# Kernel tuning notes

Measured on AMD Instinct MI355X. Metric: run time of the kernel, lower is better.

Reference implementation:

```python
import jax, jax.numpy as jnp
import numpy as np

N_NODES = 4096
NUM_GRAPHS = 16
NODE_DIM = 8
EDGE_DIM = 4
HID = 128
N_WIRES = 9  # 3 edge wires + 4 node wires (center=3) + 2 ancillas
SEL_LAYERS = 1
PI = np.pi


def _c(x):
    return x.astype(jnp.complex64)


def _ry(t):
    c, s = _c(jnp.cos(t / 2)), _c(jnp.sin(t / 2))
    return jnp.stack([jnp.stack([c, -s], -1), jnp.stack([s, c], -1)], -2)


def _rx(t):
    c, s = _c(jnp.cos(t / 2)), -1j * _c(jnp.sin(t / 2))
    return jnp.stack([jnp.stack([c, s], -1), jnp.stack([s, c], -1)], -2)


def _rz(t):
    e = jnp.exp(-0.5j * _c(t))
    z = jnp.zeros_like(e)
    return jnp.stack([jnp.stack([e, z], -1), jnp.stack([z, jnp.conj(e)], -1)], -2)


def _rot(phi, theta, omega):  # qml.Rot = RZ(omega) @ RY(theta) @ RZ(phi)
    return _rz(omega) @ _ry(theta) @ _rz(phi)


def _ctrl(U):  # block-diag(I2, U)
    b = U.shape[:-2]
    I = jnp.broadcast_to(jnp.eye(2, dtype=jnp.complex64), b + (2, 2))
    Z = jnp.zeros(b + (2, 2), jnp.complex64)
    return jnp.concatenate([jnp.concatenate([I, Z], -1), jnp.concatenate([Z, U], -1)], -2)


_CNOT = jnp.array([[1, 0, 0, 0], [0, 1, 0, 0], [0, 0, 0, 1], [0, 0, 1, 0]], jnp.complex64)


def _apply1(state, U, w):  # state [S, 2**9], U [2,2] or [S,2,2]
    S = state.shape[0]
    s = jnp.moveaxis(state.reshape((S,) + (2,) * N_WIRES), 1 + w, 1)
    out = jnp.einsum('bij,bjk->bik', jnp.broadcast_to(U, (S, 2, 2)), s.reshape(S, 2, -1))
    return jnp.moveaxis(out.reshape(s.shape), 1, 1 + w).reshape(S, -1)


def _apply2(state, U, w1, w2):  # U [4,4] or [S,4,4], wire order (w1,w2)
    S = state.shape[0]
    s = jnp.moveaxis(state.reshape((S,) + (2,) * N_WIRES), (1 + w1, 1 + w2), (1, 2))
    out = jnp.einsum('bij,bjk->bik', jnp.broadcast_to(U, (S, 4, 4)), s.reshape(S, 4, -1))
    return jnp.moveaxis(out.reshape(s.shape), (1, 2), (1 + w1, 1 + w2)).reshape(S, -1)


def _sel(state, weights, wires):  # qml.StronglyEntanglingLayers, weights [L, n, 3]->here [L,3,3]
    L, n = weights.shape[0], len(wires)
    for l in range(L):
        for j, w in enumerate(wires):
            state = _apply1(state, _rot(weights[l, j, 0], weights[l, j, 1], weights[l, j, 2]), w)
        r = l % (n - 1) + 1
        for j in range(n):
            state = _apply2(state, _CNOT, wires[j], wires[(j + r) % n])
    return state


def _pqc(inputs, strong, inits, update):
    # inputs: [S, 7, 2] angles (rows 0..2 edge feats, rows 3..6 node feats, center node = row 3)
    S = inputs.shape[0]
    state = jnp.zeros((S, 2 ** N_WIRES), jnp.complex64).at[:, 0].set(1.0)
    for i in range(3):
        state = _apply1(state, _ry(inputs[:, i, 0]), i)
        state = _apply1(state, _rz(inputs[:, i, 1]), i)
    for i in range(4):
        state = _apply1(state, _ry(inputs[:, 3 + i, 0]), 3 + i)
        state = _apply1(state, _rz(inputs[:, 3 + i, 1]), 3 + i)
    for i in range(3):  # message_passing_pqc per edge
        e, nb, a1, a2 = i, 4 + i, 7, 8
        state = _apply2(state, _ctrl(_rx(inits[0, 0])), nb, a1)
        state = _apply2(state, _ctrl(_ry(inits[0, 1])), e, a1)
        state = _apply2(state, _ctrl(_rz(inits[0, 2])), nb, a2)
        state = _apply2(state, _ctrl(_ry(inits[0, 3])), e, a2)
        state = _sel(state, strong[0], [e, nb, a1])
        state = _sel(state, strong[1], [a1, nb, a2])
    state = _sel(state, update, [3, 7, 8])
    # expval(PauliX) on center wire 3: wires 0..2 -> 8, wire 3 -> 2, wires 4..8 -> 32
    s = state.reshape(S, 8, 2, 32)
    return 2.0 * jnp.real(jnp.sum(jnp.conj(s[:, :, 0]) * s[:, :, 1], axis=(1, 2)))


def _mlp(x, W1, b1, W2, b2):  # PyG MLP, act between layers, dropout in eval = identity
    return jax.nn.leaky_relu(x @ W1 + b1) @ W2 + b2


def _forward(node_feat, edge_attr, Wn1, bn1, Wn2, bn2, We1, be1, We2, be2,
             strong, inits, update, Wu1, bu1, Wu2, bu2, Wh1, bh1, Wh2, bh2,
             subgraphs, edge_ids, batch):
    x = jnp.tanh(_mlp(node_feat, Wn1, bn1, Wn2, bn2)) * PI   # input_process
    e = jnp.tanh(_mlp(edge_attr, We1, be1, We2, be2)) * PI
    q_in = jnp.concatenate([e[edge_ids], x[subgraphs]], axis=1)  # [S,3,2]+[S,4,2] -> [S,7,2]
    aggr = _pqc(q_in, strong, inits, update)[:, None]            # [S,1]
    centers = subgraphs[:, 0]
    upd = _mlp(jnp.concatenate([x[centers], aggr], axis=-1), Wu1, bu1, Wu2, bu2)  # [S,2]
    x = x + jnp.zeros_like(x).at[centers].add(upd)               # index_add + residual
    gsum = jax.ops.segment_sum(x, batch, num_segments=NUM_GRAPHS)
    gcnt = jax.ops.segment_sum(jnp.ones((x.shape[0], 1), x.dtype), batch, num_segments=NUM_GRAPHS)
    g = gsum / gcnt                                              # global_mean_pool
    return _mlp(g, Wh1, bh1, Wh2, bh2)


def setup_inputs() -> dict:
    key = jax.random.key(0)
    ks = jax.random.split(key, 16)
    N, G = N_NODES, NUM_GRAPHS
    node_feat = jax.random.normal(ks[0], (N, NODE_DIM), jnp.float32)
    edge_attr = jax.random.normal(ks[1], (3 * N, EDGE_DIM), jnp.float32)
    i = np.arange(N)
    # star subgraph per node: center i with ring neighbors i+1,i+2,i+3 (mod N);
    # edge (i, i+k) has id 3*i + (k-1) in edge_attr (idx_dict materialized).
    subgraphs = jnp.asarray(np.stack([i, (i + 1) % N, (i + 2) % N, (i + 3) % N], 1), jnp.int32)
    edge_ids = jnp.asarray(np.stack([3 * i, 3 * i + 1, 3 * i + 2], 1), jnp.int32)
    batch = jnp.asarray(i // (N // G), jnp.int32)

    def lin(k, fan_in, shape):
        return jax.random.uniform(k, shape, jnp.float32, -1.0, 1.0) / np.sqrt(fan_in)

    def qw(k, shape):  # uniform_pi_init
        return jax.random.uniform(k, shape, jnp.float32, 0.0, PI)

    k = jax.random.split(ks[2], 24)
    return {
        'node_feat': node_feat, 'edge_attr': edge_attr,
        'Wn1': lin(k[0], NODE_DIM, (NODE_DIM, HID)), 'bn1': lin(k[1], NODE_DIM, (HID,)),
        'Wn2': lin(k[2], HID, (HID, 2)), 'bn2': lin(k[3], HID, (2,)),
        'We1': lin(k[4], EDGE_DIM, (EDGE_DIM, HID)), 'be1': lin(k[5], EDGE_DIM, (HID,)),
        'We2': lin(k[6], HID, (HID, 2)), 'be2': lin(k[7], HID, (2,)),
        'strong': qw(k[8], (2, SEL_LAYERS, 3, 3)), 'inits': qw(k[9], (1, 4)),
        'update': qw(k[10], (SEL_LAYERS, 3, 3)),
        'Wu1': lin(k[11], 3, (3, HID)), 'bu1': lin(k[12], 3, (HID,)),
        'Wu2': lin(k[13], HID, (HID, 2)), 'bu2': lin(k[14], HID, (2,)),
        'Wh1': lin(k[15], 2, (2, 2)), 'bh1': lin(k[16], 2, (2,)),
        'Wh2': lin(k[17], 2, (2, 2)), 'bh2': lin(k[18], 2, (2,)),
        'subgraphs': subgraphs, 'edge_ids': edge_ids, 'batch': batch,
    }


def reference(node_feat, edge_attr, Wn1, bn1, Wn2, bn2, We1, be1, We2, be2,
              strong, inits, update, Wu1, bu1, Wu2, bu2, Wh1, bh1, Wh2, bh2,
              subgraphs, edge_ids, batch):
    return _forward(node_feat, edge_attr, Wn1, bn1, Wn2, bn2, We1, be1, We2, be2,
                    strong, inits, update, Wu1, bu1, Wu2, bu2, Wh1, bh1, Wh2, bh2,
                    subgraphs, edge_ids, batch)
```

## Files before the change

kernel.cpp:

```cpp
#include <hip/hip_runtime.h>
#include <math.h>

#define PI_F 3.14159265358979323846f

__device__ __forceinline__ float2 cmul2(float2 a, float2 b) {
    return make_float2(a.x * b.x - a.y * b.y, a.x * b.y + a.y * b.x);
}
__device__ __forceinline__ float2 cmac2(float2 u, float2 a, float2 v, float2 b) {
    float2 r;
    r.x = u.x * a.x - u.y * a.y + v.x * b.x - v.y * b.y;
    r.y = u.x * a.y + u.y * a.x + v.x * b.y + v.y * b.x;
    return r;
}

struct M4 { float2 u00, u01, u10, u11; };

__device__ __forceinline__ M4 mmul4(const M4& A, const M4& B) {
    M4 R;
    R.u00 = cmac2(A.u00, B.u00, A.u01, B.u10);
    R.u01 = cmac2(A.u00, B.u01, A.u01, B.u11);
    R.u10 = cmac2(A.u10, B.u00, A.u11, B.u10);
    R.u11 = cmac2(A.u10, B.u01, A.u11, B.u11);
    return R;
}
__device__ __forceinline__ M4 mry(float t) {
    float c = cosf(0.5f * t), s = sinf(0.5f * t);
    M4 R; R.u00 = {c, 0}; R.u01 = {-s, 0}; R.u10 = {s, 0}; R.u11 = {c, 0};
    return R;
}
__device__ __forceinline__ M4 mrz(float t) {
    float c = cosf(0.5f * t), s = sinf(0.5f * t);
    M4 R; R.u00 = {c, -s}; R.u01 = {0, 0}; R.u10 = {0, 0}; R.u11 = {c, s};
    return R;
}
__device__ __forceinline__ M4 mrx(float t) {
    float c = cosf(0.5f * t), s = sinf(0.5f * t);
    M4 R; R.u00 = {c, 0}; R.u01 = {0, -s}; R.u10 = {0, -s}; R.u11 = {c, 0};
    return R;
}
__device__ __forceinline__ M4 mrot(float phi, float th, float om) {
    return mmul4(mmul4(mrz(om), mry(th)), mrz(phi));
}

__device__ __forceinline__ float2 shflx(float2 v, int mask) {
    return make_float2(__shfl_xor(v.x, mask, 64), __shfl_xor(v.y, mask, 64));
}

__device__ __forceinline__ M4 ldm(const float* __restrict__ g) {
    M4 M;
    M.u00 = make_float2(g[0], g[1]); M.u01 = make_float2(g[2], g[3]);
    M.u10 = make_float2(g[4], g[5]); M.u11 = make_float2(g[6], g[7]);
    return M;
}


template <int TB>
__device__ __forceinline__ void rot_reg(const M4& U, float2 (&amp)[8]) {
#pragma unroll
    for (int r = 0; r < 8; r++)
        if (((r >> TB) & 1) == 0) {
            int r1 = r | (1 << TB);
            float2 a = amp[r], b = amp[r1];
            amp[r]  = cmac2(U.u00, a, U.u01, b);
            amp[r1] = cmac2(U.u10, a, U.u11, b);
        }
}

template <int LB>
__device__ __forceinline__ void rot_lane(const M4& U, float2 (&amp)[8], int lane) {
    bool hi = (lane >> LB) & 1;
    float2 cA = hi ? U.u11 : U.u00;
    float2 cB = hi ? U.u10 : U.u01;
#pragma unroll
    for (int r = 0; r < 8; r++) {
        float2 o = shflx(amp[r], 1 << LB);
        amp[r] = cmac2(cA, amp[r], cB, o);
    }
}

template <int WIRE>
__device__ __forceinline__ void rot1(const M4& U, float2 (&amp)[8], int lane) {
    constexpr int BIT = 8 - WIRE;
    if constexpr (BIT < 3) rot_reg<BIT>(U, amp);
    else rot_lane<BIT - 3>(U, amp, lane);
}

template <int CW, int TW>
__device__ __forceinline__ void crot(const M4& U, float2 (&amp)[8], int lane) {
    constexpr int CBIT = 8 - CW, TBIT = 8 - TW;
    static_assert(TBIT < 3, "controlled targets are reg bits here");
    if constexpr (CBIT >= 3) {
        bool c = (lane >> (CBIT - 3)) & 1;
        M4 E;
        E.u00 = c ? U.u00 : make_float2(1.f, 0.f);
        E.u01 = c ? U.u01 : make_float2(0.f, 0.f);
        E.u10 = c ? U.u10 : make_float2(0.f, 0.f);
        E.u11 = c ? U.u11 : make_float2(1.f, 0.f);
        rot_reg<TBIT>(E, amp);
    } else {
#pragma unroll
        for (int r = 0; r < 8; r++)
            if (((r >> CBIT) & 1) == 1 && ((r >> TBIT) & 1) == 0) {
                int r1 = r | (1 << TBIT);
                float2 a = amp[r], b = amp[r1];
                amp[r]  = cmac2(U.u00, a, U.u01, b);
                amp[r1] = cmac2(U.u10, a, U.u11, b);
            }
    }
}

template <int CW, int TW>
__device__ __forceinline__ void cnotg(float2 (&amp)[8], int lane) {
    constexpr int CBIT = 8 - CW, TBIT = 8 - TW;
    if constexpr (CBIT < 3 && TBIT < 3) {
#pragma unroll
        for (int r = 0; r < 8; r++)
            if (((r >> CBIT) & 1) == 1 && ((r >> TBIT) & 1) == 0) {
                int r1 = r | (1 << TBIT);
                float2 t = amp[r]; amp[r] = amp[r1]; amp[r1] = t;
            }
    } else if constexpr (CBIT >= 3 && TBIT < 3) {
        bool c = (lane >> (CBIT - 3)) & 1;
#pragma unroll
        for (int r = 0; r < 8; r++)
            if (((r >> TBIT) & 1) == 0) {
                int r1 = r | (1 << TBIT);
                float2 t0 = amp[r], t1 = amp[r1];
                amp[r]  = c ? t1 : t0;
                amp[r1] = c ? t0 : t1;
            }
    } else if constexpr (CBIT < 3 && TBIT >= 3) {
#pragma unroll
        for (int r = 0; r < 8; r++)
            if (((r >> CBIT) & 1) == 1) {
                amp[r] = shflx(amp[r], 1 << (TBIT - 3));
            }
    } else {
        bool c = (lane >> (CBIT - 3)) & 1;
#pragma unroll
        for (int r = 0; r < 8; r++) {
            float2 o = shflx(amp[r], 1 << (TBIT - 3));
            amp[r] = c ? o : amp[r];
        }
    }
}

template <int W0, int W1, int W2>
__device__ __forceinline__ void sel3m(const float* __restrict__ gm, float2 (&amp)[8], int lane) {
    rot1<W0>(ldm(gm),      amp, lane);
    rot1<W1>(ldm(gm + 8),  amp, lane);
    rot1<W2>(ldm(gm + 16), amp, lane);
    cnotg<W0, W1>(amp, lane);
    cnotg<W1, W2>(amp, lane);
    cnotg<W2, W0>(amp, lane);
}

template <int I>
__device__ __forceinline__ void block_i(float2 (&amp)[8], const M4& crx, const M4& cry1,
                                        const M4& crz, const M4& cry2,
                                        const float* __restrict__ gm, int lane) {
    constexpr int EW = I, NB = 4 + I;
    crot<NB, 7>(crx,  amp, lane);
    crot<EW, 7>(cry1, amp, lane);
    crot<NB, 8>(crz,  amp, lane);
    crot<EW, 8>(cry2, amp, lane);
    sel3m<EW, NB, 7>(gm + 32, amp, lane);
    sel3m<7, NB, 8>(gm + 56,  amp, lane);
}


__global__ void prep_kernel(const float* __restrict__ strong, const float* __restrict__ inits,
                            const float* __restrict__ update, float* __restrict__ gm) {
    int j = threadIdx.x;
    if (j >= 13) return;
    M4 M;
    if (j == 0)      M = mrx(inits[0]);
    else if (j == 1) M = mry(inits[1]);
    else if (j == 2) M = mrz(inits[2]);
    else if (j == 3) M = mry(inits[3]);
    else if (j < 7)  { const float* w = strong + (j - 4) * 3;     M = mrot(w[0], w[1], w[2]); }
    else if (j < 10) { const float* w = strong + 9 + (j - 7) * 3; M = mrot(w[0], w[1], w[2]); }
    else             { const float* w = update + (j - 10) * 3;    M = mrot(w[0], w[1], w[2]); }
    float* o = gm + j * 8;
    o[0] = M.u00.x; o[1] = M.u00.y; o[2] = M.u01.x; o[3] = M.u01.y;
    o[4] = M.u10.x; o[5] = M.u10.y; o[6] = M.u11.x; o[7] = M.u11.y;
}

__global__ __launch_bounds__(256) void mlp_both_kernel(
        const float* __restrict__ node_feat, const float* __restrict__ edge_attr,
        const float* __restrict__ Wn1, const float* __restrict__ bn1,
        const float* __restrict__ Wn2, const float* __restrict__ bn2,
        const float* __restrict__ We1, const float* __restrict__ be1,
        const float* __restrict__ We2, const float* __restrict__ be2,
        float* __restrict__ x, float* __restrict__ e,
        int N, int NE, int nodeBlocks) {
    if ((int)blockIdx.x < nodeBlocks) {
        int r = blockIdx.x * 256 + threadIdx.x;
        if (r >= N) return;
        float f[8];
#pragma unroll
        for (int k = 0; k < 8; k++) f[k] = node_feat[r * 8 + k];
        float o0 = bn2[0], o1 = bn2[1];
        for (int j = 0; j < 128; j++) {
            float h = bn1[j];
#pragma unroll
            for (int k = 0; k < 8; k++) h += f[k] * Wn1[k * 128 + j];
            h = h > 0.f ? h : 0.01f * h;
            o0 += h * Wn2[j * 2 + 0];
            o1 += h * Wn2[j * 2 + 1];
        }
        x[r * 2 + 0] = tanhf(o0) * PI_F;
        x[r * 2 + 1] = tanhf(o1) * PI_F;
    } else {
        int r = (blockIdx.x - nodeBlocks) * 256 + threadIdx.x;
        if (r >= NE) return;
        float f[4];
#pragma unroll
        for (int k = 0; k < 4; k++) f[k] = edge_attr[r * 4 + k];
        float o0 = be2[0], o1 = be2[1];
        for (int j = 0; j < 128; j++) {
            float h = be1[j];
#pragma unroll
            for (int k = 0; k < 4; k++) h += f[k] * We1[k * 128 + j];
            h = h > 0.f ? h : 0.01f * h;
            o0 += h * We2[j * 2 + 0];
            o1 += h * We2[j * 2 + 1];
        }
        e[r * 2 + 0] = tanhf(o0) * PI_F;
        e[r * 2 + 1] = tanhf(o1) * PI_F;
    }
}

__global__ __launch_bounds__(256) void pqc_kernel(
        const float* __restrict__ x, const float* __restrict__ e,
        const int* __restrict__ subgraphs, const int* __restrict__ edge_ids,
        const float* __restrict__ gm, float* __restrict__ aggr, int ntot) {
    int wave = threadIdx.x >> 6;
    int lane = threadIdx.x & 63;
    int s = blockIdx.x * 4 + wave;
    if (s >= ntot) return;

    float ang[7][2];
    for (int j = 0; j < 3; j++) {
        int eid = edge_ids[s * 3 + j];
        ang[j][0] = e[2 * eid]; ang[j][1] = e[2 * eid + 1];
    }
    for (int j = 0; j < 4; j++) {
        int nid = subgraphs[s * 4 + j];
        ang[3 + j][0] = x[2 * nid]; ang[3 + j][1] = x[2 * nid + 1];
    }

    float2 c = make_float2(1.f, 0.f);
#pragma unroll
    for (int w = 0; w < 6; w++) {
        float a = 0.5f * ang[w][0], b = 0.5f * ang[w][1];
        float ca = __cosf(a), sa = __sinf(a);
        float cb = __cosf(b), sb = __sinf(b);
        float2 v0 = make_float2(ca * cb, -ca * sb);
        float2 v1 = make_float2(sa * cb,  sa * sb);
        int bit = (lane >> (5 - w)) & 1;
        c = cmul2(c, bit ? v1 : v0);
    }
    float2 amp[8];
#pragma unroll
    for (int r = 0; r < 8; r++) amp[r] = make_float2(0.f, 0.f);
    {
        float a = 0.5f * ang[6][0], b = 0.5f * ang[6][1];
        float ca = __cosf(a), sa = __sinf(a);
        float cb = __cosf(b), sb = __sinf(b);
        amp[0] = cmul2(c, make_float2(ca * cb, -ca * sb));
        amp[4] = cmul2(c, make_float2(sa * cb,  sa * sb));
    }

    M4 crx  = ldm(gm);
    M4 cry1 = ldm(gm + 8);
    M4 crz  = ldm(gm + 16);
    M4 cry2 = ldm(gm + 24);

    block_i<0>(amp, crx, cry1, crz, cry2, gm, lane);
    block_i<1>(amp, crx, cry1, crz, cry2, gm, lane);
    block_i<2>(amp, crx, cry1, crz, cry2, gm, lane);
    sel3m<3, 7, 8>(gm + 80, amp, lane);

    float acc = 0.f;
#pragma unroll
    for (int r = 0; r < 8; r++) {
        float2 o = shflx(amp[r], 4);
        acc += amp[r].x * o.x + amp[r].y * o.y;
    }
    for (int off = 32; off > 0; off >>= 1) acc += __shfl_down(acc, off, 64);
    if (lane == 0) aggr[s] = acc;
}

__global__ void upd_kernel(const float* __restrict__ x, const float* __restrict__ aggr,
                           const int* __restrict__ subgraphs,
                           const float* __restrict__ W1, const float* __restrict__ b1,
                           const float* __restrict__ W2, const float* __restrict__ b2,
                           float* __restrict__ xadd, int rows) {
    int r = blockIdx.x * blockDim.x + threadIdx.x;
    if (r >= rows) return;
    int c = subgraphs[r * 4];
    float f0 = x[2 * c], f1 = x[2 * c + 1], f2 = aggr[r];
    float o0 = b2[0], o1 = b2[1];
    for (int j = 0; j < 128; j++) {
        float h = b1[j] + f0 * W1[j] + f1 * W1[128 + j] + f2 * W1[256 + j];
        h = h > 0.f ? h : 0.01f * h;
        o0 += h * W2[j * 2 + 0];
        o1 += h * W2[j * 2 + 1];
    }
    atomicAdd(&xadd[2 * c + 0], o0);
    atomicAdd(&xadd[2 * c + 1], o1);
}

#define MAX_GRAPHS 64
__global__ __launch_bounds__(256) void pool_kernel(
        const float* __restrict__ x, const float* __restrict__ xadd,
        const int* __restrict__ batch,
        float* __restrict__ gsum, float* __restrict__ gcnt, int rows, int ngraphs) {
    __shared__ float bins[3 * MAX_GRAPHS];
    for (int i = threadIdx.x; i < 3 * ngraphs; i += blockDim.x) bins[i] = 0.f;
    __syncthreads();

    int r = blockIdx.x * blockDim.x + threadIdx.x;
    int lane = threadIdx.x & 63;
    bool active = r < rows;
    int b = 0; float v0 = 0.f, v1 = 0.f, cc = 0.f;
    if (active) {
        b = batch[r];
        v0 = x[2 * r + 0] + xadd[2 * r + 0];
        v1 = x[2 * r + 1] + xadd[2 * r + 1];
        cc = 1.f;
    }
    int b0 = __shfl(b, 0);
    bool uni = __all(active && b == b0);
    if (uni) {
        for (int off = 32; off > 0; off >>= 1) {
            v0 += __shfl_down(v0, off);
            v1 += __shfl_down(v1, off);
        }
        if (lane == 0) {
            atomicAdd(&bins[3 * b0 + 0], v0);
            atomicAdd(&bins[3 * b0 + 1], v1);
            atomicAdd(&bins[3 * b0 + 2], 64.f);
        }
    } else if (active) {
        atomicAdd(&bins[3 * b + 0], v0);
        atomicAdd(&bins[3 * b + 1], v1);
        atomicAdd(&bins[3 * b + 2], cc);
    }
    __syncthreads();

    for (int i = threadIdx.x; i < ngraphs; i += blockDim.x) {
        float s0 = bins[3 * i + 0], s1 = bins[3 * i + 1], sc = bins[3 * i + 2];
        if (s0 != 0.f || s1 != 0.f || sc != 0.f) {
            atomicAdd(&gsum[2 * i + 0], s0);
            atomicAdd(&gsum[2 * i + 1], s1);
            atomicAdd(&gcnt[i], sc);
        }
    }
}

__global__ void head_kernel(const float* __restrict__ gsum, const float* __restrict__ gcnt,
                            const float* __restrict__ Wh1, const float* __restrict__ bh1,
                            const float* __restrict__ Wh2, const float* __restrict__ bh2,
                            float* __restrict__ out, int ngraphs) {
    int g = threadIdx.x;
    if (g >= ngraphs) return;
    float c = gcnt[g];
    float g0 = gsum[2 * g + 0] / c;
    float g1 = gsum[2 * g + 1] / c;
    float h0 = g0 * Wh1[0] + g1 * Wh1[2] + bh1[0];
    float h1 = g0 * Wh1[1] + g1 * Wh1[3] + bh1[1];
    h0 = h0 > 0.f ? h0 : 0.01f * h0;
    h1 = h1 > 0.f ? h1 : 0.01f * h1;
    out[2 * g + 0] = h0 * Wh2[0] + h1 * Wh2[2] + bh2[0];
    out[2 * g + 1] = h0 * Wh2[1] + h1 * Wh2[3] + bh2[1];
}

extern "C" void kernel_launch(void* const* d_in, const int* in_sizes, int n_in,
                              void* d_out, int out_size, void* d_ws, size_t ws_size,
                              hipStream_t stream) {
    const float* node_feat = (const float*)d_in[0];
    const float* edge_attr = (const float*)d_in[1];
    const float* Wn1 = (const float*)d_in[2];
    const float* bn1 = (const float*)d_in[3];
    const float* Wn2 = (const float*)d_in[4];
    const float* bn2 = (const float*)d_in[5];
    const float* We1 = (const float*)d_in[6];
    const float* be1 = (const float*)d_in[7];
    const float* We2 = (const float*)d_in[8];
    const float* be2 = (const float*)d_in[9];
    const float* strong = (const float*)d_in[10];
    const float* inits  = (const float*)d_in[11];
    const float* update = (const float*)d_in[12];
    const float* Wu1 = (const float*)d_in[13];
    const float* bu1 = (const float*)d_in[14];
    const float* Wu2 = (const float*)d_in[15];
    const float* bu2 = (const float*)d_in[16];
    const float* Wh1 = (const float*)d_in[17];
    const float* bh1 = (const float*)d_in[18];
    const float* Wh2 = (const float*)d_in[19];
    const float* bh2 = (const float*)d_in[20];
    const int* subgraphs = (const int*)d_in[21];
    const int* edge_ids  = (const int*)d_in[22];
    const int* batch     = (const int*)d_in[23];

    const int N  = in_sizes[0] / 8;
    const int NE = in_sizes[1] / 4;
    const int NG = out_size / 2;

    float* ws   = (float*)d_ws;
    float* x    = ws;
    float* e    = x + (size_t)N * 2;
    float* aggr = e + (size_t)NE * 2;
    float* xadd = aggr + N;
    float* gsum = xadd + (size_t)N * 2;
    float* gcnt = gsum + (size_t)NG * 2;
    float* gm   = gcnt + NG;

    hipMemsetAsync(xadd, 0, (size_t)(N * 2 + NG * 3) * sizeof(float), stream);

    prep_kernel<<<1, 64, 0, stream>>>(strong, inits, update, gm);

    int nodeBlocks = (N + 255) / 256;
    int edgeBlocks = (NE + 255) / 256;
    mlp_both_kernel<<<nodeBlocks + edgeBlocks, 256, 0, stream>>>(
        node_feat, edge_attr, Wn1, bn1, Wn2, bn2, We1, be1, We2, be2, x, e, N, NE, nodeBlocks);

    pqc_kernel<<<(N + 3) / 4, 256, 0, stream>>>(x, e, subgraphs, edge_ids, gm, aggr, N);

    upd_kernel<<<(N + 255) / 256, 256, 0, stream>>>(x, aggr, subgraphs, Wu1, bu1, Wu2, bu2, xadd, N);
    pool_kernel<<<(N + 255) / 256, 256, 0, stream>>>(x, xadd, batch, gsum, gcnt, N, NG);
    head_kernel<<<1, 64, 0, stream>>>(gsum, gcnt, Wh1, bh1, Wh2, bh2, (float*)d_out, NG);
}
```

Baseline: 162.7 us.

## Fuse update MLP into pooling, specialize controlled rotations, fold memset into prep

The separate update kernel that scattered into an xadd buffer is merged into the pooling kernel, which now adds each row's update output straight into the graph bin of its center node. This removes the xadd buffer, one launch and the memset. The small zeroing of gsum/gcnt moves into prep_kernel. Controlled RX/RY/RZ gates now use specialized real cos/sin arithmetic instead of generic complex 2x2 matrices, which cuts FLOPs in the PQC kernel. The fused path relies on the center node being in the same graph for the warp-uniform fast path; otherwise it falls back to per-thread shared atomics.

Measured after the change: 151.2 us. -7.0%, faster.

```diff
diff --git a/kernel.cpp b/kernel.cpp
--- a/kernel.cpp
+++ b/kernel.cpp
@@ -33,11 +33,6 @@
     M4 R; R.u00 = {c, -s}; R.u01 = {0, 0}; R.u10 = {0, 0}; R.u11 = {c, s};
     return R;
 }
-__device__ __forceinline__ M4 mrx(float t) {
-    float c = cosf(0.5f * t), s = sinf(0.5f * t);
-    M4 R; R.u00 = {c, 0}; R.u01 = {0, -s}; R.u10 = {0, -s}; R.u11 = {c, 0};
-    return R;
-}
 __device__ __forceinline__ M4 mrot(float phi, float th, float om) {
     return mmul4(mmul4(mrz(om), mry(th)), mrz(phi));
 }
@@ -85,26 +80,78 @@
     else rot_lane<BIT - 3>(U, amp, lane);
 }
 
-template <int CW, int TW>
-__device__ __forceinline__ void crot(const M4& U, float2 (&amp)[8], int lane) {
-    constexpr int CBIT = 8 - CW, TBIT = 8 - TW;
-    static_assert(TBIT < 3, "controlled targets are reg bits here");
+
+template <int CBIT, int TB>
+__device__ __forceinline__ void crx_g(float c, float s, float2 (&amp)[8], int lane) {
     if constexpr (CBIT >= 3) {
-        bool c = (lane >> (CBIT - 3)) & 1;
-        M4 E;
-        E.u00 = c ? U.u00 : make_float2(1.f, 0.f);
-        E.u01 = c ? U.u01 : make_float2(0.f, 0.f);
-        E.u10 = c ? U.u10 : make_float2(0.f, 0.f);
-        E.u11 = c ? U.u11 : make_float2(1.f, 0.f);
-        rot_reg<TBIT>(E, amp);
+        bool ct = (lane >> (CBIT - 3)) & 1;
+        float cc = ct ? c : 1.f, ss = ct ? s : 0.f;
+#pragma unroll
+        for (int r = 0; r < 8; r++)
+            if (((r >> TB) & 1) == 0) {
+                int r1 = r | (1 << TB);
+                float2 a = amp[r], b = amp[r1];
+                amp[r]  = make_float2(cc * a.x + ss * b.y, cc * a.y - ss * b.x);
+                amp[r1] = make_float2(ss * a.y + cc * b.x, cc * b.y - ss * a.x);
+            }
     } else {
 #pragma unroll
         for (int r = 0; r < 8; r++)
-            if (((r >> CBIT) & 1) == 1 && ((r >> TBIT) & 1) == 0) {
-                int r1 = r | (1 << TBIT);
-                float2 a = amp[r], b = amp[r1];
-                amp[r]  = cmac2(U.u00, a, U.u01, b);
-                amp[r1] = cmac2(U.u10, a, U.u11, b);
+            if (((r >> CBIT) & 1) == 1 && ((r >> TB) & 1) == 0) {
+                int r1 = r | (1 << TB);
+                float2 a = amp[r], b = amp[r1];
+                amp[r]  = make_float2(c * a.x + s * b.y, c * a.y - s * b.x);
+                amp[r1] = make_float2(s * a.y + c * b.x, c * b.y - s * a.x);
+            }
+    }
+}
+
+template <int CBIT, int TB>
+__device__ __forceinline__ void cry_g(float c, float s, float2 (&amp)[8], int lane) {
+    if constexpr (CBIT >= 3) {
+        bool ct = (lane >> (CBIT - 3)) & 1;
+        float cc = ct ? c : 1.f, ss = ct ? s : 0.f;
+#pragma unroll
+        for (int r = 0; r < 8; r++)
+            if (((r >> TB) & 1) == 0) {
+                int r1 = r | (1 << TB);
+                float2 a = amp[r], b = amp[r1];
+                amp[r]  = make_float2(cc * a.x - ss * b.x, cc * a.y - ss * b.y);
+                amp[r1] = make_float2(ss * a.x + cc * b.x, ss * a.y + cc * b.y);
+            }
+    } else {
+#pragma unroll
+        for (int r = 0; r < 8; r++)
+            if (((r >> CBIT) & 1) == 1 && ((r >> TB) & 1) == 0) {
+                int r1 = r | (1 << TB);
+                float2 a = amp[r], b = amp[r1];
+                amp[r]  = make_float2(c * a.x - s * b.x, c * a.y - s * b.y);
+                amp[r1] = make_float2(s * a.x + c * b.x, s * a.y + c * b.y);
+            }
+    }
+}
+
+template <int CBIT, int TB>
+__device__ __forceinline__ void crz_g(float c, float s, float2 (&amp)[8], int lane) {
+    if constexpr (CBIT >= 3) {
+        bool ct = (lane >> (CBIT - 3)) & 1;
+        float cc = ct ? c : 1.f, ss = ct ? s : 0.f;
+#pragma unroll
+        for (int r = 0; r < 8; r++)
+            if (((r >> TB) & 1) == 0) {
+                int r1 = r | (1 << TB);
+                float2 a = amp[r], b = amp[r1];
+                amp[r]  = make_float2(cc * a.x + ss * a.y, cc * a.y - ss * a.x);
+                amp[r1] = make_float2(cc * b.x - ss * b.y, cc * b.y + ss * b.x);
+            }
+    } else {
+#pragma unroll
+        for (int r = 0; r < 8; r++)
+            if (((r >> CBIT) & 1) == 1 && ((r >> TB) & 1) == 0) {
+                int r1 = r | (1 << TB);
+                float2 a = amp[r], b = amp[r1];
+                amp[r]  = make_float2(c * a.x + s * a.y, c * a.y - s * a.x);
+                amp[r1] = make_float2(c * b.x - s * b.y, c * b.y + s * b.x);
             }
     }
 }
@@ -156,34 +203,36 @@
 }
 
 template <int I>
-__device__ __forceinline__ void block_i(float2 (&amp)[8], const M4& crx, const M4& cry1,
-                                        const M4& crz, const M4& cry2,
+__device__ __forceinline__ void block_i(float2 (&amp)[8], float cx, float sx, float cy1, float sy1,
+                                        float cz, float sz, float cy2, float sy2,
                                         const float* __restrict__ gm, int lane) {
-    constexpr int EW = I, NB = 4 + I;
-    crot<NB, 7>(crx,  amp, lane);
-    crot<EW, 7>(cry1, amp, lane);
-    crot<NB, 8>(crz,  amp, lane);
-    crot<EW, 8>(cry2, amp, lane);
-    sel3m<EW, NB, 7>(gm + 32, amp, lane);
-    sel3m<7, NB, 8>(gm + 56,  amp, lane);
+    crx_g<4 - I, 1>(cx,  sx,  amp, lane);
+    cry_g<8 - I, 1>(cy1, sy1, amp, lane);
+    crz_g<4 - I, 0>(cz,  sz,  amp, lane);
+    cry_g<8 - I, 0>(cy2, sy2, amp, lane);
+    sel3m<I, 4 + I, 7>(gm + 8,  amp, lane);
+    sel3m<7, 4 + I, 8>(gm + 32, amp, lane);
 }
 
 
 __global__ void prep_kernel(const float* __restrict__ strong, const float* __restrict__ inits,
-                            const float* __restrict__ update, float* __restrict__ gm) {
+                            const float* __restrict__ update, float* __restrict__ gm,
+                            float* __restrict__ zbuf, int nzero) {
     int j = threadIdx.x;
-    if (j >= 13) return;
-    M4 M;
-    if (j == 0)      M = mrx(inits[0]);
-    else if (j == 1) M = mry(inits[1]);
-    else if (j == 2) M = mrz(inits[2]);
-    else if (j == 3) M = mry(inits[3]);
-    else if (j < 7)  { const float* w = strong + (j - 4) * 3;     M = mrot(w[0], w[1], w[2]); }
-    else if (j < 10) { const float* w = strong + 9 + (j - 7) * 3; M = mrot(w[0], w[1], w[2]); }
-    else             { const float* w = update + (j - 10) * 3;    M = mrot(w[0], w[1], w[2]); }
-    float* o = gm + j * 8;
-    o[0] = M.u00.x; o[1] = M.u00.y; o[2] = M.u01.x; o[3] = M.u01.y;
-    o[4] = M.u10.x; o[5] = M.u10.y; o[6] = M.u11.x; o[7] = M.u11.y;
+    if (j < 4) {
+        gm[2 * j]     = cosf(0.5f * inits[j]);
+        gm[2 * j + 1] = sinf(0.5f * inits[j]);
+    } else if (j < 13) {
+        const float* w;
+        if (j < 7)       w = strong + (j - 4) * 3;
+        else if (j < 10) w = strong + 9 + (j - 7) * 3;
+        else             w = update + (j - 10) * 3;
+        M4 M = mrot(w[0], w[1], w[2]);
+        float* o = gm + 8 + (j - 4) * 8;
+        o[0] = M.u00.x; o[1] = M.u00.y; o[2] = M.u01.x; o[3] = M.u01.y;
+        o[4] = M.u10.x; o[5] = M.u10.y; o[6] = M.u11.x; o[7] = M.u11.y;
+    }
+    for (int i = j; i < nzero; i += 64) zbuf[i] = 0.f;
 }
 
 __global__ __launch_bounds__(256) void mlp_both_kernel(
@@ -272,15 +321,15 @@
         amp[4] = cmul2(c, make_float2(sa * cb,  sa * sb));
     }
 
-    M4 crx  = ldm(gm);
-    M4 cry1 = ldm(gm + 8);
-    M4 crz  = ldm(gm + 16);
-    M4 cry2 = ldm(gm + 24);
-
-    block_i<0>(amp, crx, cry1, crz, cry2, gm, lane);
-    block_i<1>(amp, crx, cry1, crz, cry2, gm, lane);
-    block_i<2>(amp, crx, cry1, crz, cry2, gm, lane);
-    sel3m<3, 7, 8>(gm + 80, amp, lane);
+    float cx  = gm[0], sx  = gm[1];
+    float cy1 = gm[2], sy1 = gm[3];
+    float cz  = gm[4], sz  = gm[5];
+    float cy2 = gm[6], sy2 = gm[7];
+
+    block_i<0>(amp, cx, sx, cy1, sy1, cz, sz, cy2, sy2, gm, lane);
+    block_i<1>(amp, cx, sx, cy1, sy1, cz, sz, cy2, sy2, gm, lane);
+    block_i<2>(amp, cx, sx, cy1, sy1, cz, sz, cy2, sy2, gm, lane);
+    sel3m<3, 7, 8>(gm + 56, amp, lane);
 
     float acc = 0.f;
 #pragma unroll
@@ -292,30 +341,12 @@
     if (lane == 0) aggr[s] = acc;
 }
 
-__global__ void upd_kernel(const float* __restrict__ x, const float* __restrict__ aggr,
-                           const int* __restrict__ subgraphs,
-                           const float* __restrict__ W1, const float* __restrict__ b1,
-                           const float* __restrict__ W2, const float* __restrict__ b2,
-                           float* __restrict__ xadd, int rows) {
-    int r = blockIdx.x * blockDim.x + threadIdx.x;
-    if (r >= rows) return;
-    int c = subgraphs[r * 4];
-    float f0 = x[2 * c], f1 = x[2 * c + 1], f2 = aggr[r];
-    float o0 = b2[0], o1 = b2[1];
-    for (int j = 0; j < 128; j++) {
-        float h = b1[j] + f0 * W1[j] + f1 * W1[128 + j] + f2 * W1[256 + j];
-        h = h > 0.f ? h : 0.01f * h;
-        o0 += h * W2[j * 2 + 0];
-        o1 += h * W2[j * 2 + 1];
-    }
-    atomicAdd(&xadd[2 * c + 0], o0);
-    atomicAdd(&xadd[2 * c + 1], o1);
-}
-
 #define MAX_GRAPHS 64
-__global__ __launch_bounds__(256) void pool_kernel(
-        const float* __restrict__ x, const float* __restrict__ xadd,
-        const int* __restrict__ batch,
+__global__ __launch_bounds__(256) void pool_upd_kernel(
+        const float* __restrict__ x, const float* __restrict__ aggr,
+        const int* __restrict__ subgraphs, const int* __restrict__ batch,
+        const float* __restrict__ W1, const float* __restrict__ b1,
+        const float* __restrict__ W2, const float* __restrict__ b2,
         float* __restrict__ gsum, float* __restrict__ gcnt, int rows, int ngraphs) {
     __shared__ float bins[3 * MAX_GRAPHS];
     for (int i = threadIdx.x; i < 3 * ngraphs; i += blockDim.x) bins[i] = 0.f;
@@ -324,29 +355,42 @@
     int r = blockIdx.x * blockDim.x + threadIdx.x;
     int lane = threadIdx.x & 63;
     bool active = r < rows;
-    int b = 0; float v0 = 0.f, v1 = 0.f, cc = 0.f;
+    int b = 0, bc = 0;
+    float v0 = 0.f, v1 = 0.f, o0 = 0.f, o1 = 0.f;
     if (active) {
         b = batch[r];
-        v0 = x[2 * r + 0] + xadd[2 * r + 0];
-        v1 = x[2 * r + 1] + xadd[2 * r + 1];
-        cc = 1.f;
+        v0 = x[2 * r + 0];
+        v1 = x[2 * r + 1];
+        int cidx = subgraphs[r * 4];
+        bc = batch[cidx];
+        float f0 = x[2 * cidx], f1 = x[2 * cidx + 1], f2 = aggr[r];
+        o0 = b2[0]; o1 = b2[1];
+        for (int j = 0; j < 128; j++) {
+            float h = b1[j] + f0 * W1[j] + f1 * W1[128 + j] + f2 * W1[256 + j];
+            h = h > 0.f ? h : 0.01f * h;
+            o0 += h * W2[j * 2 + 0];
+            o1 += h * W2[j * 2 + 1];
+        }
     }
     int b0 = __shfl(b, 0);
-    bool uni = __all(active && b == b0);
+    bool uni = __all(active && b == b0 && bc == b0);
     if (uni) {
+        float s0 = v0 + o0, s1 = v1 + o1;
         for (int off = 32; off > 0; off >>= 1) {
-            v0 += __shfl_down(v0, off);
-            v1 += __shfl_down(v1, off);
+            s0 += __shfl_down(s0, off);
+            s1 += __shfl_down(s1, off);
         }
         if (lane == 0) {
-            atomicAdd(&bins[3 * b0 + 0], v0);
-            atomicAdd(&bins[3 * b0 + 1], v1);
+            atomicAdd(&bins[3 * b0 + 0], s0);
+            atomicAdd(&bins[3 * b0 + 1], s1);
             atomicAdd(&bins[3 * b0 + 2], 64.f);
         }
     } else if (active) {
         atomicAdd(&bins[3 * b + 0], v0);
         atomicAdd(&bins[3 * b + 1], v1);
-        atomicAdd(&bins[3 * b + 2], cc);
+        atomicAdd(&bins[3 * b + 2], 1.f);
+        atomicAdd(&bins[3 * bc + 0], o0);
+        atomicAdd(&bins[3 * bc + 1], o1);
     }
     __syncthreads();
 
@@ -413,14 +457,11 @@
     float* x    = ws;
     float* e    = x + (size_t)N * 2;
     float* aggr = e + (size_t)NE * 2;
-    float* xadd = aggr + N;
-    float* gsum = xadd + (size_t)N * 2;
+    float* gsum = aggr + N;
     float* gcnt = gsum + (size_t)NG * 2;
     float* gm   = gcnt + NG;
 
-    hipMemsetAsync(xadd, 0, (size_t)(N * 2 + NG * 3) * sizeof(float), stream);
-
-    prep_kernel<<<1, 64, 0, stream>>>(strong, inits, update, gm);
+    prep_kernel<<<1, 64, 0, stream>>>(strong, inits, update, gm, gsum, 3 * NG);
 
     int nodeBlocks = (N + 255) / 256;
     int edgeBlocks = (NE + 255) / 256;
@@ -429,7 +470,8 @@
 
     pqc_kernel<<<(N + 3) / 4, 256, 0, stream>>>(x, e, subgraphs, edge_ids, gm, aggr, N);
 
-    upd_kernel<<<(N + 255) / 256, 256, 0, stream>>>(x, aggr, subgraphs, Wu1, bu1, Wu2, bu2, xadd, N);
-    pool_kernel<<<(N + 255) / 256, 256, 0, stream>>>(x, xadd, batch, gsum, gcnt, N, NG);
+    pool_upd_kernel<<<(N + 255) / 256, 256, 0, stream>>>(
+        x, aggr, subgraphs, batch, Wu1, bu1, Wu2, bu2, gsum, gcnt, N, NG);
+
     head_kernel<<<1, 64, 0, stream>>>(gsum, gcnt, Wh1, bh1, Wh2, bh2, (float*)d_out, NG);
 }
```
